# Performance work log

Measured on AMD Instinct MI355X. Metric: run time of the kernel, lower is better.

The kernel has to match this reference:

```python
import jax, jax.numpy as jnp
import numpy as np
import math

B, S, D, H = 4, 2048, 1024, 16
HD = D // H  # head dim = 64


def _rope_tables(seq_len, dim, base=10000.0):
    half = dim // 2
    inv_freq = 1.0 / (base ** (jnp.arange(half, dtype=jnp.float32) / half))
    angles = jnp.arange(seq_len, dtype=jnp.float32)[:, None] * inv_freq[None, :]  # [S, half]
    return jnp.cos(angles), jnp.sin(angles)


def _apply_rope(x, cos, sin):
    # x: [B,H,S,HD]; half-split rotation (non-interleaved)
    half = x.shape[-1] // 2
    x1, x2 = x[..., :half], x[..., half:]
    c = cos[None, None, :, :]
    s = sin[None, None, :, :]
    return jnp.concatenate([x1 * c - x2 * s, x1 * s + x2 * c], axis=-1)


def setup_inputs() -> dict:
    key = jax.random.key(0)
    ks = jax.random.split(key, 7)
    sc = 1.0 / math.sqrt(D)
    return {
        "Q": jax.random.normal(ks[0], (B, S, D), jnp.float32),
        "K": jax.random.normal(ks[1], (B, S, D), jnp.float32),
        "V": jax.random.normal(ks[2], (B, S, D), jnp.float32),
        "Wq": jax.random.normal(ks[3], (D, D), jnp.float32) * sc,
        "bq": jnp.zeros((D,), jnp.float32),
        "Wk": jax.random.normal(ks[4], (D, D), jnp.float32) * sc,
        "bk": jnp.zeros((D,), jnp.float32),
        "Wv": jax.random.normal(ks[5], (D, D), jnp.float32) * sc,
        "bv": jnp.zeros((D,), jnp.float32),
        "Wo": jax.random.normal(ks[6], (D, D), jnp.float32) * sc,
        "bo": jnp.zeros((D,), jnp.float32),
    }


def reference(Q, K, V, Wq, bq, Wk, bk, Wv, bv, Wo, bo):
    bs, n, _ = Q.shape
    # projections (torch Linear: x @ W.T + b)
    q = (Q @ Wq.T + bq).reshape(bs, n, H, HD).transpose(0, 2, 1, 3)  # [B,H,S,HD]
    k = (K @ Wk.T + bk).reshape(bs, n, H, HD).transpose(0, 2, 1, 3)
    v = (V @ Wv.T + bv).reshape(bs, n, H, HD).transpose(0, 2, 1, 3)
    cos, sin = _rope_tables(n, HD)
    q = _apply_rope(q, cos, sin)
    k = _apply_rope(k, cos, sin)
    scores = jnp.einsum('bhqd,bhkd->bhqk', q, k) / math.sqrt(HD)
    causal = jnp.tril(jnp.ones((n, n), dtype=bool))
    scores = jnp.where(causal[None, None], scores, -jnp.inf)
    probs = jax.nn.softmax(scores, axis=-1)
    out = jnp.einsum('bhqk,bhkd->bhqd', probs, v)  # [B,H,S,HD]
    out = out.transpose(0, 2, 1, 3).reshape(bs, n, D)
    return out @ Wo.T + bo
```

## Files before the change

kernel.cpp:

```cpp
#include <hip/hip_runtime.h>
#include <hip/hip_bf16.h>

#define BB 4
#define SS 2048
#define DDIM 1024
#define HH 16
#define MTOT (BB*SS)

typedef __attribute__((ext_vector_type(8))) __bf16 bf16x8;
typedef __attribute__((ext_vector_type(4))) float f32x4;

static __device__ __forceinline__ unsigned short f2bf(float f) {
  union { float f; unsigned u; } v; v.f = f;
  unsigned r = v.u + 0x7FFFu + ((v.u >> 16) & 1u);
  return (unsigned short)(r >> 16);
}

static __device__ __forceinline__ bf16x8 ld_bf16x8(const void* p) {
  bf16x8 r;
  __builtin_memcpy(&r, p, 16);
  return r;
}

static __device__ __forceinline__ void gload_lds16(const void* g, void* l) {
  __builtin_amdgcn_global_load_lds(
      (const __attribute__((address_space(1))) unsigned int*)g,
      (__attribute__((address_space(3))) unsigned int*)l, 16, 0, 0);
}

__global__ void k_rope_tables(float2* __restrict__ t) {
  int i = blockIdx.x * 256 + threadIdx.x;
  int s = i >> 5, d = i & 31;
  float inv = powf(10000.0f, -((float)d) / 32.0f);
  float a = (float)s * inv;
  t[i] = make_float2(cosf(a), sinf(a));
}

__global__ void k_cvt_bf16(const float* __restrict__ in,
                           unsigned short* __restrict__ out, int n4) {
  int i = blockIdx.x * 256 + threadIdx.x;
  if (i >= n4) return;
  float4 v = ((const float4*)in)[i];
  ushort4 o;
  o.x = f2bf(v.x); o.y = f2bf(v.y); o.z = f2bf(v.z); o.w = f2bf(v.w);
  ((ushort4*)out)[i] = o;
}

#define E_ROPE 0
#define E_VT   1
#define E_F32  2

template<int EPI>
__global__ __launch_bounds__(256, 3) void k_gemm(
    const unsigned short* __restrict__ A,
    const unsigned short* __restrict__ Bw,
    const float* __restrict__ bias,
    void* __restrict__ out,
    const float2* __restrict__ tcs,
    float scale)
{
  __shared__ unsigned short As[128*64];
  __shared__ unsigned short Bs[128*64];
  const int tid  = threadIdx.x;
  const int lane = tid & 63;
  const int wv   = tid >> 6;
  const int wr   = wv >> 1, wc = wv & 1;
  const int l15  = lane & 15, l4 = lane >> 4;
  const int bm0  = blockIdx.x * 128;
  const int bn0  = blockIdx.y * 128;

  const f32x4 fz = {0.f, 0.f, 0.f, 0.f};
  f32x4 acc[4][4];
#pragma unroll
  for (int m = 0; m < 4; ++m)
#pragma unroll
    for (int n = 0; n < 4; ++n) acc[m][n] = fz;

  const int srow = lane >> 3;
  const int scol = ((lane & 7) ^ srow) * 8;

  for (int kt = 0; kt < 16; ++kt) {
    const int k0 = kt * 64;
#pragma unroll
    for (int i = 0; i < 4; ++i) {
      const int c = wv * 4 + i;
      const int row = c * 8 + srow;
      gload_lds16(A  + (size_t)(bm0 + row) * 1024 + k0 + scol, (char*)As + c * 1024);
      gload_lds16(Bw + (size_t)(bn0 + row) * 1024 + k0 + scol, (char*)Bs + c * 1024);
    }
    __syncthreads();
#pragma unroll
    for (int h = 0; h < 2; ++h) {
      bf16x8 af[4], bfr[4];
#pragma unroll
      for (int m = 0; m < 4; ++m) {
        const int row = 64 * wr + 16 * m + l15;
        const int sl = ((l4 + 4 * h) ^ (l15 & 7)) * 8;
        af[m] = ld_bf16x8(&As[row * 64 + sl]);
      }
#pragma unroll
      for (int n = 0; n < 4; ++n) {
        const int row = 64 * wc + 16 * n + l15;
        const int sl = ((l4 + 4 * h) ^ (l15 & 7)) * 8;
        bfr[n] = ld_bf16x8(&Bs[row * 64 + sl]);
      }
#pragma unroll
      for (int m = 0; m < 4; ++m)
#pragma unroll
        for (int n = 0; n < 4; ++n)
          acc[m][n] = __builtin_amdgcn_mfma_f32_16x16x32_bf16(af[m], bfr[n], acc[m][n], 0, 0, 0);
    }
    __syncthreads();
  }

  if (EPI == E_ROPE) {
    unsigned short* O = (unsigned short*)out;
#pragma unroll
    for (int m = 0; m < 4; ++m) {
      const int row0 = bm0 + 64 * wr + 16 * m + 4 * l4;
#pragma unroll
      for (int n = 0; n < 2; ++n) {
        const int d = 16 * n + l15;
        const int col1 = bn0 + 64 * wc + d;
        const float b1 = bias[col1], b2 = bias[col1 + 32];
#pragma unroll
        for (int i = 0; i < 4; ++i) {
          const int row = row0 + i;
          const int s = row & (SS - 1);
          const float2 cs = tcs[s * 32 + d];
          const float x1 = acc[m][n][i] + b1;
          const float x2 = acc[m][n + 2][i] + b2;
          O[(size_t)row * 1024 + col1]      = f2bf((x1 * cs.x - x2 * cs.y) * scale);
          O[(size_t)row * 1024 + col1 + 32] = f2bf((x1 * cs.y + x2 * cs.x) * scale);
        }
      }
    }
  } else if (EPI == E_VT) {
    unsigned short* O = (unsigned short*)out;
    const int hh = (bn0 + 64 * wc) >> 6;
#pragma unroll
    for (int m = 0; m < 4; ++m) {
      const int row0 = bm0 + 64 * wr + 16 * m + 4 * l4;
      const int b_ = row0 >> 11;
      const int s0 = row0 & (SS - 1);
#pragma unroll
      for (int n = 0; n < 4; ++n) {
        const int d = 16 * n + l15;
        const float bb = bias[bn0 + 64 * wc + d];
        ushort4 o;
        o.x = f2bf(acc[m][n][0] + bb);
        o.y = f2bf(acc[m][n][1] + bb);
        o.z = f2bf(acc[m][n][2] + bb);
        o.w = f2bf(acc[m][n][3] + bb);
        *(ushort4*)&O[((size_t)(b_ * HH + hh) * 64 + d) * SS + s0] = o;
      }
    }
  } else {
    float* O = (float*)out;
#pragma unroll
    for (int m = 0; m < 4; ++m) {
      const int row0 = bm0 + 64 * wr + 16 * m + 4 * l4;
#pragma unroll
      for (int n = 0; n < 4; ++n) {
        const int col = bn0 + 64 * wc + 16 * n + l15;
        const float bb = bias[col];
#pragma unroll
        for (int i = 0; i < 4; ++i)
          O[(size_t)(row0 + i) * 1024 + col] = acc[m][n][i] + bb;
      }
    }
  }
}

__global__ __launch_bounds__(256, 4) void k_attn(
    const unsigned short* __restrict__ qr,
    const unsigned short* __restrict__ kr,
    const unsigned short* __restrict__ vT,
    unsigned short* __restrict__ ao)
{
  __shared__ unsigned short Ks[2][64*64];
  __shared__ unsigned short Vs[2][64*64];
  __shared__ unsigned short Ps[4][16*64];
  const int tid = threadIdx.x, lane = tid & 63, wv = tid >> 6;
  const int l15 = lane & 15, l4 = lane >> 4;
  const int bh = blockIdx.x & 63;
  const int pair = blockIdx.x >> 6;
  const int b_ = bh >> 4, h_ = bh & 15;

  const int srow = lane >> 3;
  const int scol = ((lane & 7) ^ srow) * 8;

  const f32x4 fz = {0.f, 0.f, 0.f, 0.f};

  for (int half = 0; half < 2; ++half) {
    const int j = half ? (31 - pair) : pair;
    const int q0 = j * 64;

    const size_t qoff = ((size_t)(b_ * SS + q0 + 16 * wv + l15)) * 1024 + h_ * 64 + l4 * 8;
    const bf16x8 aq0 = ld_bf16x8(&qr[qoff]);
    const bf16x8 aq1 = ld_bf16x8(&qr[qoff + 32]);

    f32x4 accO[4];
#pragma unroll
    for (int dt = 0; dt < 4; ++dt) accO[dt] = fz;
    float mrun[4], lrun[4];
#pragma unroll
    for (int i = 0; i < 4; ++i) { mrun[i] = -1e30f; lrun[i] = 0.f; }

    {
#pragma unroll
      for (int i = 0; i < 2; ++i) {
        const int c = wv * 2 + i;
        const int row = c * 8 + srow;
        gload_lds16(kr + ((size_t)(b_ * SS + row)) * 1024 + h_ * 64 + scol,
                    (char*)&Ks[0][0] + c * 1024);
        gload_lds16(vT + ((size_t)(bh * 64 + row)) * SS + scol,
                    (char*)&Vs[0][0] + c * 1024);
      }
    }
    __syncthreads();

    int cur = 0;
    for (int kt = 0; kt <= j; ++kt) {
      if (kt < j) {
        const int k0 = (kt + 1) * 64;
        const int nb = cur ^ 1;
#pragma unroll
        for (int i = 0; i < 2; ++i) {
          const int c = wv * 2 + i;
          const int row = c * 8 + srow;
          gload_lds16(kr + ((size_t)(b_ * SS + k0 + row)) * 1024 + h_ * 64 + scol,
                      (char*)&Ks[nb][0] + c * 1024);
          gload_lds16(vT + ((size_t)(bh * 64 + row)) * SS + k0 + scol,
                      (char*)&Vs[nb][0] + c * 1024);
        }
      }

      const bool diag = (kt == j);
      f32x4 sc[4];
      __builtin_amdgcn_s_setprio(1);
#pragma unroll
      for (int n = 0; n < 4; ++n) {
        if (!diag || n <= wv) {
          const int row = 16 * n + l15;
          const int sl0 = ((l4 + 0) ^ (l15 & 7)) * 8;
          const int sl1 = ((l4 + 4) ^ (l15 & 7)) * 8;
          bf16x8 kf0 = ld_bf16x8(&Ks[cur][row * 64 + sl0]);
          bf16x8 kf1 = ld_bf16x8(&Ks[cur][row * 64 + sl1]);
          sc[n] = __builtin_amdgcn_mfma_f32_16x16x32_bf16(aq0, kf0, fz, 0, 0, 0);
          sc[n] = __builtin_amdgcn_mfma_f32_16x16x32_bf16(aq1, kf1, sc[n], 0, 0, 0);
        } else {
          sc[n] = fz;
        }
      }
      __builtin_amdgcn_s_setprio(0);
      if (diag) {
#pragma unroll
        for (int n = 0; n < 4; ++n)
#pragma unroll
          for (int i = 0; i < 4; ++i) {
            const int kj = 16 * n + l15;
            const int qi = 16 * wv + 4 * l4 + i;
            if (kj > qi) sc[n][i] = -1e30f;
          }
      }

      float tmax[4];
#pragma unroll
      for (int i = 0; i < 4; ++i) {
        float t = fmaxf(fmaxf(fmaxf(sc[0][i], sc[1][i]), sc[2][i]), sc[3][i]);
        t = fmaxf(t, __shfl_xor(t, 1));
        t = fmaxf(t, __shfl_xor(t, 2));
        t = fmaxf(t, __shfl_xor(t, 4));
        t = fmaxf(t, __shfl_xor(t, 8));
        tmax[i] = t;
      }
      bool need = (tmax[0] > mrun[0] + 11.f) | (tmax[1] > mrun[1] + 11.f) |
                  (tmax[2] > mrun[2] + 11.f) | (tmax[3] > mrun[3] + 11.f);
      if (__any(need)) {
#pragma unroll
        for (int i = 0; i < 4; ++i) {
          const float mn = fmaxf(mrun[i], tmax[i]);
          const float alpha = exp2f(mrun[i] - mn);
          mrun[i] = mn;
          lrun[i] *= alpha;
#pragma unroll
          for (int dt = 0; dt < 4; ++dt) accO[dt][i] *= alpha;
        }
      }
      float pn[4][4];
#pragma unroll
      for (int i = 0; i < 4; ++i) {
        float rs = 0.f;
#pragma unroll
        for (int n = 0; n < 4; ++n) { pn[n][i] = exp2f(sc[n][i] - mrun[i]); rs += pn[n][i]; }
        rs += __shfl_xor(rs, 1);
        rs += __shfl_xor(rs, 2);
        rs += __shfl_xor(rs, 4);
        rs += __shfl_xor(rs, 8);
        lrun[i] += rs;
      }
#pragma unroll
      for (int n = 0; n < 4; ++n)
#pragma unroll
        for (int i = 0; i < 4; ++i) {
          const int r = 4 * l4 + i;
          const int cc = 16 * n + l15;
          const int phys = (cc >> 3) ^ (r & 7);
          Ps[wv][r * 64 + phys * 8 + (cc & 7)] = f2bf(pn[n][i]);
        }
      __builtin_amdgcn_s_setprio(1);
#pragma unroll
      for (int kk = 0; kk < 2; ++kk) {
        if (diag && wv < 2 && kk == 1) continue;
        const int psl = ((l4 + 4 * kk) ^ (l15 & 7)) * 8;
        bf16x8 pa = ld_bf16x8(&Ps[wv][l15 * 64 + psl]);
#pragma unroll
        for (int dt = 0; dt < 4; ++dt) {
          const int row = 16 * dt + l15;
          const int vsl = ((l4 + 4 * kk) ^ (l15 & 7)) * 8;
          bf16x8 vb = ld_bf16x8(&Vs[cur][row * 64 + vsl]);
          accO[dt] = __builtin_amdgcn_mfma_f32_16x16x32_bf16(pa, vb, accO[dt], 0, 0, 0);
        }
      }
      __builtin_amdgcn_s_setprio(0);
      __syncthreads();
      cur ^= 1;
    }

#pragma unroll
    for (int i = 0; i < 4; ++i) {
      const float inv = 1.0f / lrun[i];
      const size_t row = (size_t)(b_ * SS + q0 + 16 * wv + 4 * l4 + i);
#pragma unroll
      for (int dt = 0; dt < 4; ++dt)
        ao[row * 1024 + h_ * 64 + 16 * dt + l15] = f2bf(accO[dt][i] * inv);
    }
  }
}

extern "C" void kernel_launch(void* const* d_in, const int* in_sizes, int n_in,
                              void* d_out, int out_size, void* d_ws, size_t ws_size,
                              hipStream_t stream) {
  const float* Q  = (const float*)d_in[0];
  const float* K  = (const float*)d_in[1];
  const float* V  = (const float*)d_in[2];
  const float* Wq = (const float*)d_in[3];
  const float* bq = (const float*)d_in[4];
  const float* Wk = (const float*)d_in[5];
  const float* bk = (const float*)d_in[6];
  const float* Wv = (const float*)d_in[7];
  const float* bv = (const float*)d_in[8];
  const float* Wo = (const float*)d_in[9];
  const float* bo = (const float*)d_in[10];
  float* out = (float*)d_out;

  char* ws = (char*)d_ws;
  float2* tcs = (float2*)(ws);
  unsigned short* wqb = (unsigned short*)(ws + 512 * 1024);
  unsigned short* wkb = wqb + (1u << 20);
  unsigned short* wvb = wkb + (1u << 20);
  unsigned short* wob = wvb + (1u << 20);
  unsigned short* xb  = wob + (1u << 20);
  unsigned short* qrb = xb  + (size_t)MTOT * 1024;
  unsigned short* krb = qrb + (size_t)MTOT * 1024;
  unsigned short* vtb = krb + (size_t)MTOT * 1024;
  unsigned short* aob = vtb + (size_t)MTOT * 1024;

  k_rope_tables<<<256, 256, 0, stream>>>(tcs);
  k_cvt_bf16<<<1024, 256, 0, stream>>>(Wq, wqb, 1024 * 1024 / 4);
  k_cvt_bf16<<<1024, 256, 0, stream>>>(Wk, wkb, 1024 * 1024 / 4);
  k_cvt_bf16<<<1024, 256, 0, stream>>>(Wv, wvb, 1024 * 1024 / 4);
  k_cvt_bf16<<<1024, 256, 0, stream>>>(Wo, wob, 1024 * 1024 / 4);

  dim3 gg(MTOT / 128, 8);
  const float qsc = 0.125f * 1.4426950408889634f;

  k_cvt_bf16<<<MTOT * 1024 / 4 / 256, 256, 0, stream>>>(Q, xb, MTOT * 1024 / 4);
  k_gemm<E_ROPE><<<gg, 256, 0, stream>>>(xb, wqb, bq, qrb, tcs, qsc);
  k_cvt_bf16<<<MTOT * 1024 / 4 / 256, 256, 0, stream>>>(K, xb, MTOT * 1024 / 4);
  k_gemm<E_ROPE><<<gg, 256, 0, stream>>>(xb, wkb, bk, krb, tcs, 1.0f);
  k_cvt_bf16<<<MTOT * 1024 / 4 / 256, 256, 0, stream>>>(V, xb, MTOT * 1024 / 4);
  k_gemm<E_VT><<<gg, 256, 0, stream>>>(xb, wvb, bv, vtb, tcs, 1.0f);

  k_attn<<<64 * 16, 256, 0, stream>>>(qrb, krb, vtb, aob);

  k_gemm<E_F32><<<gg, 256, 0, stream>>>(aob, wob, bo, out, tcs, 1.0f);
}
```

Measured before the change: 378.7 us.

## Use wave-wide softmax max, MFMA row sums, and truncating bf16 conversion

Replaces the per-row running max with a single max over the whole wave's score tile, taken with a full 64-lane shuffle reduction, so the rescale decision and alpha are scalar per wave. The row-sum shuffle reduction is dropped. Row sums come instead from an extra MFMA of the probability fragment against a vector of ones, which also keeps the denominator consistent with the bf16 probabilities used for P·V. The bf16 conversion of probabilities now truncates instead of rounding. This removes VALU and cross-lane work in the softmax. It risks underflow or lost precision when rows within a wave have very different maxima, and truncation adds a small bias.

```diff
diff --git a/kernel.cpp b/kernel.cpp
--- a/kernel.cpp
+++ b/kernel.cpp
@@ -191,6 +191,9 @@
   const int scol = ((lane & 7) ^ srow) * 8;
 
   const f32x4 fz = {0.f, 0.f, 0.f, 0.f};
+  bf16x8 ones;
+#pragma unroll
+  for (int j = 0; j < 8; ++j) ones[j] = (__bf16)1.0f;
 
   for (int half = 0; half < 2; ++half) {
     const int j = half ? (31 - pair) : pair;
@@ -203,9 +206,8 @@
     f32x4 accO[4];
 #pragma unroll
     for (int dt = 0; dt < 4; ++dt) accO[dt] = fz;
-    float mrun[4], lrun[4];
-#pragma unroll
-    for (int i = 0; i < 4; ++i) { mrun[i] = -1e30f; lrun[i] = 0.f; }
+    f32x4 lacc = fz;
+    float mrun = -1e30f;
 
     {
 #pragma unroll
@@ -265,49 +267,34 @@
           }
       }
 
-      float tmax[4];
-#pragma unroll
-      for (int i = 0; i < 4; ++i) {
-        float t = fmaxf(fmaxf(fmaxf(sc[0][i], sc[1][i]), sc[2][i]), sc[3][i]);
-        t = fmaxf(t, __shfl_xor(t, 1));
-        t = fmaxf(t, __shfl_xor(t, 2));
-        t = fmaxf(t, __shfl_xor(t, 4));
-        t = fmaxf(t, __shfl_xor(t, 8));
-        tmax[i] = t;
-      }
-      bool need = (tmax[0] > mrun[0] + 11.f) | (tmax[1] > mrun[1] + 11.f) |
-                  (tmax[2] > mrun[2] + 11.f) | (tmax[3] > mrun[3] + 11.f);
-      if (__any(need)) {
+      float t = sc[0][0];
+#pragma unroll
+      for (int n = 0; n < 4; ++n)
+#pragma unroll
+        for (int i = 0; i < 4; ++i) if (n || i) t = fmaxf(t, sc[n][i]);
+      t = fmaxf(t, __shfl_xor(t, 1));
+      t = fmaxf(t, __shfl_xor(t, 2));
+      t = fmaxf(t, __shfl_xor(t, 4));
+      t = fmaxf(t, __shfl_xor(t, 8));
+      t = fmaxf(t, __shfl_xor(t, 16));
+      t = fmaxf(t, __shfl_xor(t, 32));
+      if (t > mrun + 11.f) {
+        const float alpha = exp2f(mrun - t);
+        mrun = t;
+        lacc *= alpha;
+#pragma unroll
+        for (int dt = 0; dt < 4; ++dt) accO[dt] *= alpha;
+      }
+#pragma unroll
+      for (int n = 0; n < 4; ++n)
 #pragma unroll
         for (int i = 0; i < 4; ++i) {
-          const float mn = fmaxf(mrun[i], tmax[i]);
-          const float alpha = exp2f(mrun[i] - mn);
-          mrun[i] = mn;
-          lrun[i] *= alpha;
-#pragma unroll
-          for (int dt = 0; dt < 4; ++dt) accO[dt][i] *= alpha;
-        }
-      }
-      float pn[4][4];
-#pragma unroll
-      for (int i = 0; i < 4; ++i) {
-        float rs = 0.f;
-#pragma unroll
-        for (int n = 0; n < 4; ++n) { pn[n][i] = exp2f(sc[n][i] - mrun[i]); rs += pn[n][i]; }
-        rs += __shfl_xor(rs, 1);
-        rs += __shfl_xor(rs, 2);
-        rs += __shfl_xor(rs, 4);
-        rs += __shfl_xor(rs, 8);
-        lrun[i] += rs;
-      }
-#pragma unroll
-      for (int n = 0; n < 4; ++n)
-#pragma unroll
-        for (int i = 0; i < 4; ++i) {
+          const float pv = exp2f(sc[n][i] - mrun);
           const int r = 4 * l4 + i;
           const int cc = 16 * n + l15;
           const int phys = (cc >> 3) ^ (r & 7);
-          Ps[wv][r * 64 + phys * 8 + (cc & 7)] = f2bf(pn[n][i]);
+          Ps[wv][r * 64 + phys * 8 + (cc & 7)] =
+              (unsigned short)(__float_as_uint(pv) >> 16);
         }
       __builtin_amdgcn_s_setprio(1);
 #pragma unroll
@@ -322,6 +309,7 @@
           bf16x8 vb = ld_bf16x8(&Vs[cur][row * 64 + vsl]);
           accO[dt] = __builtin_amdgcn_mfma_f32_16x16x32_bf16(pa, vb, accO[dt], 0, 0, 0);
         }
+        lacc = __builtin_amdgcn_mfma_f32_16x16x32_bf16(pa, ones, lacc, 0, 0, 0);
       }
       __builtin_amdgcn_s_setprio(0);
       __syncthreads();
@@ -330,7 +318,7 @@
 
 #pragma unroll
     for (int i = 0; i < 4; ++i) {
-      const float inv = 1.0f / lrun[i];
+      const float inv = 1.0f / lacc[i];
       const size_t row = (size_t)(b_ * SS + q0 + 16 * wv + 4 * l4 + i);
 #pragma unroll
       for (int dt = 0; dt < 4; ++dt)
```

New measurement: 341.7 us. 9.8% less time.
